# Kernel optimization log

Measured on AMD Instinct MI355X. Metric: run time of the kernel, lower is better.

Reference implementation:

```python
import jax, jax.numpy as jnp
import numpy as np

N = 4096   # out_features (rows of W)
M = 4096   # in_features (cols of W)
S_L = 2048 # Givens pairs on rows
S_R = 2048 # Givens pairs on cols
T = 8192   # tokens (batch*seq)
EPS = 1e-6


def _disjoint_pairs(key, n_feat, n_pairs):
    perm = jax.random.permutation(key, n_feat)[: 2 * n_pairs]
    return perm.reshape(n_pairs, 2).astype(jnp.int32)


def setup_inputs() -> dict:
    key = jax.random.key(0)
    ks = jax.random.split(key, 8)
    x = jax.random.normal(ks[0], (T, M), dtype=jnp.float32)
    W = 0.02 * jax.random.normal(ks[1], (N, M), dtype=jnp.float32)
    bias = jnp.zeros((N,), dtype=jnp.float32)
    theta_L = 0.002 * jax.random.normal(ks[2], (S_L,), dtype=jnp.float32)
    theta_R = 0.002 * jax.random.normal(ks[3], (S_R,), dtype=jnp.float32)
    pairs_L = _disjoint_pairs(ks[4], N, S_L)
    pairs_R = _disjoint_pairs(ks[5], M, S_R)
    ecd_log_mag = jnp.zeros((N,), dtype=jnp.float32)
    base_row_norms = jnp.linalg.norm(W, axis=1)  # [N], captured at init
    return {"x": x, "W": W, "bias": bias, "theta_L": theta_L,
            "theta_R": theta_R, "ecd_log_mag": ecd_log_mag,
            "base_row_norms": base_row_norms, "pairs_L": pairs_L,
            "pairs_R": pairs_R}


def _rotate_rows(Wm, pairs, theta):
    # Disjoint Givens rotations on rows: gather pair rows, 2x2 rotate, scatter.
    i, j = pairs[:, 0], pairs[:, 1]
    c = jnp.cos(theta)[:, None]
    s = jnp.sin(theta)[:, None]
    ri, rj = Wm[i], Wm[j]              # [S, M] gathers
    return Wm.at[i].set(c * ri - s * rj).at[j].set(s * ri + c * rj)


def _rotate_cols(Wm, pairs, theta):
    i, j = pairs[:, 0], pairs[:, 1]
    c = jnp.cos(theta)[None, :]
    s = jnp.sin(theta)[None, :]
    ci, cj = Wm[:, i], Wm[:, j]        # [N, S] gathers
    return Wm.at[:, i].set(c * ci - s * cj).at[:, j].set(s * ci + c * cj)


def reference(x, W, bias, theta_L, theta_R, ecd_log_mag, base_row_norms,
              pairs_L, pairs_R):
    # Effective weight: W_eff = G_L(theta_L) @ W @ G_R(theta_R)^T
    W_eff = _rotate_rows(_rotate_cols(W, pairs_R, theta_R), pairs_L, theta_L)
    # Magnitude (ECD) rescaling: restore base per-row norms modulated by
    # learned log-magnitudes.
    row_norms = jnp.sqrt(jnp.sum(W_eff * W_eff, axis=1) + EPS)  # [N]
    scale = base_row_norms * jnp.exp(ecd_log_mag) / row_norms   # [N]
    W_eff = W_eff * scale[:, None]
    return x @ W_eff.T + bias
```

## Files before the change

kernel.cpp:

```cpp
#include <hip/hip_runtime.h>
#include <cstdint>
#include <cstddef>

constexpr int T_N = 8192;
constexpr int MM  = 4096;
constexpr int NN  = 4096;
constexpr int S_L = 2048;
constexpr int S_R = 2048;
constexpr float EPS_ = 1e-6f;

typedef float  f32x4  __attribute__((ext_vector_type(4)));
typedef __bf16 bf16x8 __attribute__((ext_vector_type(8)));
typedef unsigned short ushort8 __attribute__((ext_vector_type(8)));

__device__ __forceinline__ unsigned short f2bf(float f) {
  unsigned int u = __float_as_uint(f);
  u += 0x7FFFu + ((u >> 16) & 1u);
  return (unsigned short)(u >> 16);
}

__global__ void init_maps(float* rowC, float* rowS, int* rowP,
                          float* colC, float* colS, int* colP) {
  int i = blockIdx.x * blockDim.x + threadIdx.x;
  if (i < NN) { rowC[i] = 1.f; rowS[i] = 0.f; rowP[i] = i; }
  if (i < MM) { colC[i] = 1.f; colS[i] = 0.f; colP[i] = i; }
}

__global__ void build_maps(const float* __restrict__ thL, const float* __restrict__ thR,
                           const int* __restrict__ prL, const int* __restrict__ prR,
                           float* rowC, float* rowS, int* rowP,
                           float* colC, float* colS, int* colP) {
  int s = blockIdx.x * blockDim.x + threadIdx.x;
  if (s < S_L) {
    int i = prL[2*s], j = prL[2*s+1];
    float c = cosf(thL[s]), sn = sinf(thL[s]);
    rowC[i] = c; rowS[i] = -sn; rowP[i] = j;
    rowC[j] = c; rowS[j] =  sn; rowP[j] = i;
  }
  if (s < S_R) {
    int i = prR[2*s], j = prR[2*s+1];
    float c = cosf(thR[s]), sn = sinf(thR[s]);
    colC[i] = c; colS[i] = -sn; colP[i] = j;
    colC[j] = c; colS[j] =  sn; colP[j] = i;
  }
}

__global__ __launch_bounds__(256) void build_weff(
    const float* __restrict__ W, const float* __restrict__ brn, const float* __restrict__ elm,
    const float* __restrict__ rowC, const float* __restrict__ rowS, const int* __restrict__ rowP,
    const float* __restrict__ colC, const float* __restrict__ colS, const int* __restrict__ colP,
    unsigned short* __restrict__ Wb)
{
  __shared__ __align__(16) float rA[MM];
  __shared__ __align__(16) float rB[MM];
  __shared__ __align__(16) float rE[MM];
  __shared__ float red[4];

  int n   = blockIdx.x;
  int tid = threadIdx.x;
  int pn  = rowP[n];
  float cl = rowC[n], sl = rowS[n];
  const float* Wn = W + (size_t)n  * MM;
  const float* Wp = W + (size_t)pn * MM;

  for (int m = tid * 4; m < MM; m += 1024) {
    *(f32x4*)&rA[m] = *(const f32x4*)&Wn[m];
    *(f32x4*)&rB[m] = *(const f32x4*)&Wp[m];
  }
  __syncthreads();

  float ss = 0.f;
  for (int m = tid; m < MM; m += 256) {
    int p = colP[m];
    float c = colC[m], s = colS[m];
    float e = cl * (c * rA[m] + s * rA[p]) + sl * (c * rB[m] + s * rB[p]);
    rE[m] = e;
    ss += e * e;
  }
  #pragma unroll
  for (int o = 32; o; o >>= 1) ss += __shfl_xor(ss, o);
  int lane = tid & 63, wid = tid >> 6;
  if (lane == 0) red[wid] = ss;
  __syncthreads();
  float tot = red[0] + red[1] + red[2] + red[3];
  float scale = brn[n] * expf(elm[n]) / sqrtf(tot + EPS_);

  for (int m = tid * 8; m < MM; m += 2048) {
    ushort8 pkt;
    #pragma unroll
    for (int q = 0; q < 8; q++) pkt[q] = f2bf(rE[m + q] * scale);
    *(ushort8*)&Wb[(size_t)n * MM + m] = pkt;
  }
}

__global__ __launch_bounds__(256) void conv_x(const float* __restrict__ x,
                                              unsigned short* __restrict__ xb) {
  const size_t total = (size_t)T_N * MM / 8;
  for (size_t i = (size_t)blockIdx.x * 256 + threadIdx.x; i < total; i += 2048ull * 256ull) {
    const float* s = x + i * 8;
    f32x4 v0 = *(const f32x4*)s;
    f32x4 v1 = *(const f32x4*)(s + 4);
    ushort8 p;
    p[0] = f2bf(v0.x); p[1] = f2bf(v0.y); p[2] = f2bf(v0.z); p[3] = f2bf(v0.w);
    p[4] = f2bf(v1.x); p[5] = f2bf(v1.y); p[6] = f2bf(v1.z); p[7] = f2bf(v1.w);
    *(ushort8*)(xb + i * 8) = p;
  }
}

typedef const __attribute__((address_space(1))) unsigned int* as1_u32p;
typedef __attribute__((address_space(3))) unsigned int* as3_u32p;

__device__ __forceinline__ void gl_lds16(const void* g, void* l) {
  __builtin_amdgcn_global_load_lds((as1_u32p)g, (as3_u32p)l, 16, 0, 0);
}

constexpr int GBM = 256, GBN = 256, GBK = 64;
constexpr int NTK = MM / GBK;
constexpr int ASLOT = GBM * GBK * 2;
constexpr int BSLOT = GBN * GBK * 2;

#define SB0() __builtin_amdgcn_sched_barrier(0)
#define LGKM(N) do { asm volatile("s_waitcnt lgkmcnt(" #N ")" ::: "memory"); \
                     SB0(); } while (0)

#define RD_BP(NI0, BB)                                                        \
  _Pragma("unroll") for (int n_ = 0; n_ < 2; ++n_)                            \
  _Pragma("unroll") for (int k_ = 0; k_ < 2; ++k_)                            \
    bf[(NI0) + n_][k_] = *(const bf16x8*)((BB) + brow0 + ((NI0) + n_) * 2048  \
                                           + ((k_ * 64 + lg * 16) ^ sw));

#define RD_AQ(DST, AB, Q)                                                     \
  _Pragma("unroll") for (int i_ = 0; i_ < 2; ++i_)                            \
  _Pragma("unroll") for (int k_ = 0; k_ < 2; ++k_)                            \
    DST[i_][k_] = *(const bf16x8*)((AB) + arow0 + ((Q) * 2 + i_) * 2048       \
                                    + ((k_ * 64 + lg * 16) ^ sw));

#define CL(AF, Q, H)                                                          \
  __builtin_amdgcn_s_setprio(1);                                              \
  _Pragma("unroll") for (int k_ = 0; k_ < 2; ++k_)                            \
  _Pragma("unroll") for (int i_ = 0; i_ < 2; ++i_)                            \
  _Pragma("unroll") for (int n_ = 0; n_ < 2; ++n_)                            \
    acc[(Q) * 2 + i_][(H) + n_] = __builtin_amdgcn_mfma_f32_16x16x32_bf16(    \
        AF[i_][k_], bf[(H) + n_][k_], acc[(Q) * 2 + i_][(H) + n_], 0, 0, 0);  \
  __builtin_amdgcn_s_setprio(0);

#define STAGE_A(KOF, SL)                                                      \
  _Pragma("unroll") for (int l_ = 0; l_ < 4; ++l_)                            \
    gl_lds16(sA + (size_t)l_ * (64 * MM) + (KOF),                             \
             ldsA + (SL) * ASLOT + dstb + l_ * 8192);
#define STAGE_B(KOF, SL)                                                      \
  _Pragma("unroll") for (int l_ = 0; l_ < 4; ++l_)                            \
    gl_lds16(sB + (size_t)l_ * (64 * MM) + (KOF),                             \
             ldsB + (SL) * BSLOT + dstb + l_ * 8192);

#define GATE4 do { asm volatile("s_waitcnt vmcnt(4)" ::: "memory");           \
                   __builtin_amdgcn_s_barrier(); } while (0)
#define GATE0 do { asm volatile("s_waitcnt vmcnt(0)" ::: "memory");           \
                   __builtin_amdgcn_s_barrier(); } while (0)
#define NOGATE do { } while (0)

#define TILE(KOF, RA, RB, WA, WB, DOB, DOA, GATE)                             \
  {                                                                           \
    const char* Ab_ = ldsA + (RA) * ASLOT;                                    \
    const char* Bb_ = ldsB + (RB) * BSLOT;                                    \
    bf16x8 bf[4][2], af0[2][2], af1[2][2], af2[2][2], af3[2][2];              \
    RD_BP(0, Bb_);                                                            \
    RD_AQ(af0, Ab_, 0);                                                       \
    SB0();                                                                    \
    RD_AQ(af1, Ab_, 1);                                                       \
    if (DOB) { STAGE_B((KOF) + GBK, WB); }                                    \
    SB0();                                                                    \
    if (DOA) { STAGE_A((KOF) + 2 * GBK, WA); }                                \
    LGKM(4);                                                                  \
    CL(af0, 0, 0);                                                   \
    RD_BP(2, Bb_);                                                            \
    LGKM(4);                                                                  \
    CL(af1, 1, 0);                                                   \
    RD_AQ(af2, Ab_, 2);                                                       \
    LGKM(4);                                                                  \
    CL(af0, 0, 2);                                                   \
    RD_AQ(af3, Ab_, 3);                                                       \
    LGKM(4);                                                                  \
    CL(af1, 1, 2);                                                   \
    CL(af2, 2, 0);                                                   \
    CL(af2, 2, 2);                                                   \
    LGKM(0);                                                                  \
    CL(af3, 3, 0);                                                   \
    CL(af3, 3, 2);                                                   \
    GATE;                                                                     \
  }

__global__ __launch_bounds__(512, 2) void gemm8(
    const unsigned short* __restrict__ xb,
    const unsigned short* __restrict__ wb,
    const float* __restrict__ bias,
    float* __restrict__ C)
{
  __shared__ __align__(16) unsigned short As[3 * GBM * GBK];
  __shared__ __align__(16) unsigned short Bs[2 * GBN * GBK];
  char* ldsA = (char*)As;
  char* ldsB = (char*)Bs;

  int bid = blockIdx.x;
  int swz = (bid & 7) * 64 + (bid >> 3);
  int tn = swz & 15, tm = swz >> 4;
  const int trow0 = tm * GBM;
  const int tcol0 = tn * GBN;

  int tid  = threadIdx.x;
  int lane = tid & 63;
  int wid  = tid >> 6;
  int wr = wid >> 2, wc = wid & 3;
  int lr = lane & 15;
  int lg = lane >> 4;
  const int sw = (lr & 7) << 4;
  const int arow0 = wr * 16384 + lr * 128;
  const int brow0 = wc * 8192  + lr * 128;

  const int r0   = tid >> 3;
  const int colg = (tid & 7) ^ (r0 & 7);
  const unsigned short* sA = xb + (size_t)(trow0 + r0) * MM + colg * 8;
  const unsigned short* sB = wb + (size_t)(tcol0 + r0) * MM + colg * 8;
  const int dstb = tid * 16;

  f32x4 acc[8][4];
  #pragma unroll
  for (int i = 0; i < 8; i++)
    #pragma unroll
    for (int j = 0; j < 4; j++) {
      f32x4 z = {0.f, 0.f, 0.f, 0.f};
      acc[i][j] = z;
    }

  STAGE_B(0, 0);
  STAGE_A(0, 0);
  SB0();
  STAGE_B(GBK, 1);
  STAGE_A(GBK, 1);
  STAGE_A(2 * GBK, 2);
  asm volatile("s_waitcnt vmcnt(12)" ::: "memory");
  __builtin_amdgcn_s_barrier();

  int kof = 0;
  #pragma unroll 1
  for (int tb = 0; tb < NTK - 4; tb += 6) {
    TILE(kof      , 0, 0, 2, 1, 1, 1, GATE4);
    TILE(kof +  64, 1, 1, 0, 0, 1, 1, GATE4);
    TILE(kof + 128, 2, 0, 1, 1, 1, 1, GATE4);
    TILE(kof + 192, 0, 1, 2, 0, 1, 1, GATE4);
    TILE(kof + 256, 1, 0, 0, 1, 1, 1, GATE4);
    TILE(kof + 320, 2, 1, 1, 0, 1, 1, GATE4);
    kof += 384;
  }
  TILE(kof      , 0, 0, 2, 1, 1, 1, GATE4);
  TILE(kof +  64, 1, 1, 0, 0, 1, 1, GATE4);
  TILE(kof + 128, 2, 0, 0, 1, 1, 0, GATE0);
  TILE(kof + 192, 0, 1, 0, 0, 0, 0, NOGATE);

  #pragma unroll
  for (int ni = 0; ni < 4; ++ni) {
    int col = tcol0 + wc * 64 + ni * 16 + lr;
    float bi = bias[col];
    #pragma unroll
    for (int mi = 0; mi < 8; ++mi) {
      int rr0 = trow0 + wr * 128 + mi * 16 + lg * 4;
      #pragma unroll
      for (int qq = 0; qq < 4; ++qq)
        C[(size_t)(rr0 + qq) * NN + col] = acc[mi][ni][qq] + bi;
    }
  }
}

constexpr int BM = 128, BN = 128, BK = 64;

__global__ __launch_bounds__(256) void gemm_fb(
    const float* __restrict__ xf,
    const unsigned short* __restrict__ wb, const float* __restrict__ bias,
    float* __restrict__ C)
{
  __shared__ __align__(16) unsigned short As2[BM * BK];
  __shared__ __align__(16) unsigned short Bs2[BN * BK];

  int bid = blockIdx.x;
  int swz = (bid & 7) * 256 + (bid >> 3);
  int tn = swz & 31;
  int tm = swz >> 5;

  int tid  = threadIdx.x;
  int lane = tid & 63;
  int wid  = tid >> 6;
  int wr = wid >> 1, wc = wid & 1;
  int lr = lane & 15;
  int lg = lane >> 4;

  f32x4 acc[4][4];
  #pragma unroll
  for (int i = 0; i < 4; i++)
    #pragma unroll
    for (int j = 0; j < 4; j++) {
      f32x4 z = {0.f, 0.f, 0.f, 0.f};
      acc[i][j] = z;
    }

  int srow = tid >> 3;
  int scol = (tid & 7) * 8;
  const size_t a_base = (size_t)(tm * BM) * MM;
  const size_t b_base = (size_t)(tn * BN) * MM;

  for (int k0 = 0; k0 < MM; k0 += BK) {
    #pragma unroll
    for (int c = 0; c < 4; c++) {
      int row = c * 32 + srow;
      gl_lds16(wb + b_base + (size_t)row * MM + k0 + scol,
               (char*)Bs2 + (c * 256 + wid * 64) * 16);
    }
    #pragma unroll
    for (int c = 0; c < 4; c++) {
      int row = c * 32 + srow;
      const float* s = xf + a_base + (size_t)row * MM + k0 + scol;
      f32x4 v0 = *(const f32x4*)s;
      f32x4 v1 = *(const f32x4*)(s + 4);
      ushort8 p;
      p[0] = f2bf(v0.x); p[1] = f2bf(v0.y); p[2] = f2bf(v0.z); p[3] = f2bf(v0.w);
      p[4] = f2bf(v1.x); p[5] = f2bf(v1.y); p[6] = f2bf(v1.z); p[7] = f2bf(v1.w);
      *(ushort8*)&As2[(c * 256 + tid) * 8] = p;
    }
    __syncthreads();

    #pragma unroll
    for (int kk = 0; kk < 2; kk++) {
      bf16x8 a[4], b[4];
      #pragma unroll
      for (int i = 0; i < 4; i++) {
        a[i] = *(const bf16x8*)&As2[(wr * 64 + i * 16 + lr) * BK + kk * 32 + lg * 8];
        b[i] = *(const bf16x8*)&Bs2[(wc * 64 + i * 16 + lr) * BK + kk * 32 + lg * 8];
      }
      #pragma unroll
      for (int i = 0; i < 4; i++)
        #pragma unroll
        for (int j = 0; j < 4; j++)
          acc[i][j] = __builtin_amdgcn_mfma_f32_16x16x32_bf16(a[i], b[j], acc[i][j], 0, 0, 0);
    }
    __syncthreads();
  }

  int gn0 = tn * BN + wc * 64;
  int gt0 = tm * BM + wr * 64;
  #pragma unroll
  for (int j = 0; j < 4; j++) {
    int gn = gn0 + j * 16 + lr;
    float bi = bias[gn];
    #pragma unroll
    for (int i = 0; i < 4; i++) {
      int t0 = gt0 + i * 16 + lg * 4;
      #pragma unroll
      for (int q = 0; q < 4; q++)
        C[(size_t)(t0 + q) * NN + gn] = acc[i][j][q] + bi;
    }
  }
}

extern "C" void kernel_launch(void* const* d_in, const int* in_sizes, int n_in,
                              void* d_out, int out_size, void* d_ws, size_t ws_size,
                              hipStream_t stream)
{
  const float* x    = (const float*)d_in[0];
  const float* W    = (const float*)d_in[1];
  const float* bias = (const float*)d_in[2];
  const float* thL  = (const float*)d_in[3];
  const float* thR  = (const float*)d_in[4];
  const float* elm  = (const float*)d_in[5];
  const float* brn  = (const float*)d_in[6];
  const int*   prL  = (const int*)d_in[7];
  const int*   prR  = (const int*)d_in[8];
  float* out = (float*)d_out;

  char* ws = (char*)d_ws;
  unsigned short* Wb = (unsigned short*)ws;
  size_t off = (size_t)NN * MM * 2;
  float* rowC = (float*)(ws + off); off += NN * 4;
  float* rowS = (float*)(ws + off); off += NN * 4;
  int*   rowP = (int*)  (ws + off); off += NN * 4;
  float* colC = (float*)(ws + off); off += MM * 4;
  float* colS = (float*)(ws + off); off += MM * 4;
  int*   colP = (int*)  (ws + off); off += MM * 4;
  unsigned short* xb = (unsigned short*)(ws + off);
  bool use_xb = ws_size >= off + (size_t)T_N * MM * 2;

  init_maps <<<16, 256, 0, stream>>>(rowC, rowS, rowP, colC, colS, colP);
  build_maps<<< 8, 256, 0, stream>>>(thL, thR, prL, prR, rowC, rowS, rowP, colC, colS, colP);
  build_weff<<<NN, 256, 0, stream>>>(W, brn, elm, rowC, rowS, rowP, colC, colS, colP, Wb);

  if (use_xb) {
    conv_x<<<2048, 256, 0, stream>>>(x, xb);
    gemm8<<<512, 512, 0, stream>>>(xb, Wb, bias, out);
  } else {
    gemm_fb<<<2048, 256, 0, stream>>>(x, Wb, bias, out);
  }
}
```

Before: 325.4 us.

## Switch bf16 GEMM to 32x32x16 MFMA tiles and drop redundant prologue loads

The main GEMM's 16x16x32 MFMA fragments become 32x32x16 MFMA fragments. The LDS read addressing, swizzle offsets, accumulator layout and epilogue store mapping are reworked to match. The larger instruction halves the MFMA issue count per tile and gives 32-wide contiguous column stores in the epilogue. The prologue no longer issues B/A stages that the first tile issues again, and the vmcnt wait is adjusted to match. It risks new LDS bank-conflict patterns from the changed swizzle and a different latency/dependency profile in the interleaved schedule.

```diff
diff --git a/kernel.cpp b/kernel.cpp
--- a/kernel.cpp
+++ b/kernel.cpp
@@ -9,8 +9,9 @@
 constexpr int S_R = 2048;
 constexpr float EPS_ = 1e-6f;
 
-typedef float  f32x4  __attribute__((ext_vector_type(4)));
-typedef __bf16 bf16x8 __attribute__((ext_vector_type(8)));
+typedef float  f32x4   __attribute__((ext_vector_type(4)));
+typedef float  f32x16  __attribute__((ext_vector_type(16)));
+typedef __bf16 bf16x8  __attribute__((ext_vector_type(8)));
 typedef unsigned short ushort8 __attribute__((ext_vector_type(8)));
 
 __device__ __forceinline__ unsigned short f2bf(float f) {
@@ -123,25 +124,20 @@
 #define LGKM(N) do { asm volatile("s_waitcnt lgkmcnt(" #N ")" ::: "memory"); \
                      SB0(); } while (0)
 
-#define RD_BP(NI0, BB)                                                        \
+#define RD_B8(BB)                                                             \
   _Pragma("unroll") for (int n_ = 0; n_ < 2; ++n_)                            \
-  _Pragma("unroll") for (int k_ = 0; k_ < 2; ++k_)                            \
-    bf[(NI0) + n_][k_] = *(const bf16x8*)((BB) + brow0 + ((NI0) + n_) * 2048  \
-                                           + ((k_ * 64 + lg * 16) ^ sw));
-
-#define RD_AQ(DST, AB, Q)                                                     \
-  _Pragma("unroll") for (int i_ = 0; i_ < 2; ++i_)                            \
-  _Pragma("unroll") for (int k_ = 0; k_ < 2; ++k_)                            \
-    DST[i_][k_] = *(const bf16x8*)((AB) + arow0 + ((Q) * 2 + i_) * 2048       \
-                                    + ((k_ * 64 + lg * 16) ^ sw));
-
-#define CL(AF, Q, H)                                                          \
+  _Pragma("unroll") for (int k_ = 0; k_ < 4; ++k_)                            \
+    bf[n_][k_] = *(const bf16x8*)((BB) + brow0 + n_ * 4096 + koff[k_]);
+
+#define RD_A4(DST, AB, MB)                                                    \
+  _Pragma("unroll") for (int k_ = 0; k_ < 4; ++k_)                            \
+    DST[k_] = *(const bf16x8*)((AB) + arow0 + (MB) * 4096 + koff[k_]);
+
+#define CL4(AF, MB, NB)                                                       \
   __builtin_amdgcn_s_setprio(1);                                              \
-  _Pragma("unroll") for (int k_ = 0; k_ < 2; ++k_)                            \
-  _Pragma("unroll") for (int i_ = 0; i_ < 2; ++i_)                            \
-  _Pragma("unroll") for (int n_ = 0; n_ < 2; ++n_)                            \
-    acc[(Q) * 2 + i_][(H) + n_] = __builtin_amdgcn_mfma_f32_16x16x32_bf16(    \
-        AF[i_][k_], bf[(H) + n_][k_], acc[(Q) * 2 + i_][(H) + n_], 0, 0, 0);  \
+  _Pragma("unroll") for (int k_ = 0; k_ < 4; ++k_)                            \
+    acc[MB][NB] = __builtin_amdgcn_mfma_f32_32x32x16_bf16(                    \
+        AF[k_], bf[NB][k_], acc[MB][NB], 0, 0, 0);                            \
   __builtin_amdgcn_s_setprio(0);
 
 #define STAGE_A(KOF, SL)                                                      \
@@ -163,30 +159,29 @@
   {                                                                           \
     const char* Ab_ = ldsA + (RA) * ASLOT;                                    \
     const char* Bb_ = ldsB + (RB) * BSLOT;                                    \
-    bf16x8 bf[4][2], af0[2][2], af1[2][2], af2[2][2], af3[2][2];              \
-    RD_BP(0, Bb_);                                                            \
-    RD_AQ(af0, Ab_, 0);                                                       \
+    bf16x8 bf[2][4], af0[4], af1[4], af2[4], af3[4];                          \
+    RD_B8(Bb_);                                                               \
+    RD_A4(af0, Ab_, 0);                                                       \
     SB0();                                                                    \
-    RD_AQ(af1, Ab_, 1);                                                       \
+    RD_A4(af1, Ab_, 1);                                                       \
+    SB0();                                                                    \
     if (DOB) { STAGE_B((KOF) + GBK, WB); }                                    \
     SB0();                                                                    \
     if (DOA) { STAGE_A((KOF) + 2 * GBK, WA); }                                \
     LGKM(4);                                                                  \
-    CL(af0, 0, 0);                                                   \
-    RD_BP(2, Bb_);                                                            \
+    CL4(af0, 0, 0);                                                           \
+    RD_A4(af2, Ab_, 2);                                                       \
     LGKM(4);                                                                  \
-    CL(af1, 1, 0);                                                   \
-    RD_AQ(af2, Ab_, 2);                                                       \
+    CL4(af1, 1, 0);                                                           \
+    CL4(af0, 0, 1);                                                           \
+    RD_A4(af3, Ab_, 3);                                                       \
     LGKM(4);                                                                  \
-    CL(af0, 0, 2);                                                   \
-    RD_AQ(af3, Ab_, 3);                                                       \
-    LGKM(4);                                                                  \
-    CL(af1, 1, 2);                                                   \
-    CL(af2, 2, 0);                                                   \
-    CL(af2, 2, 2);                                                   \
+    CL4(af2, 2, 0);                                                           \
+    CL4(af1, 1, 1);                                                           \
     LGKM(0);                                                                  \
-    CL(af3, 3, 0);                                                   \
-    CL(af3, 3, 2);                                                   \
+    CL4(af3, 3, 0);                                                           \
+    CL4(af2, 2, 1);                                                           \
+    CL4(af3, 3, 1);                                                           \
     GATE;                                                                     \
   }
 
@@ -211,11 +206,14 @@
   int lane = tid & 63;
   int wid  = tid >> 6;
   int wr = wid >> 2, wc = wid & 3;
-  int lr = lane & 15;
-  int lg = lane >> 4;
-  const int sw = (lr & 7) << 4;
-  const int arow0 = wr * 16384 + lr * 128;
-  const int brow0 = wc * 8192  + lr * 128;
+  int l31 = lane & 31;
+  int hi  = lane >> 5;
+  const int sw = (lane & 7) << 4;
+  const int arow0 = (wr * 128 + l31) * 128;
+  const int brow0 = (wc * 64  + l31) * 128;
+  int koff[4];
+  #pragma unroll
+  for (int k_ = 0; k_ < 4; ++k_) koff[k_] = (k_ * 32 + hi * 16) ^ sw;
 
   const int r0   = tid >> 3;
   const int colg = (tid & 7) ^ (r0 & 7);
@@ -223,22 +221,19 @@
   const unsigned short* sB = wb + (size_t)(tcol0 + r0) * MM + colg * 8;
   const int dstb = tid * 16;
 
-  f32x4 acc[8][4];
-  #pragma unroll
-  for (int i = 0; i < 8; i++)
-    #pragma unroll
-    for (int j = 0; j < 4; j++) {
-      f32x4 z = {0.f, 0.f, 0.f, 0.f};
-      acc[i][j] = z;
-    }
+  f32x16 acc[4][2];
+  #pragma unroll
+  for (int i = 0; i < 4; i++)
+    #pragma unroll
+    for (int j = 0; j < 2; j++)
+      #pragma unroll
+      for (int q = 0; q < 16; q++) acc[i][j][q] = 0.f;
 
   STAGE_B(0, 0);
   STAGE_A(0, 0);
   SB0();
-  STAGE_B(GBK, 1);
   STAGE_A(GBK, 1);
-  STAGE_A(2 * GBK, 2);
-  asm volatile("s_waitcnt vmcnt(12)" ::: "memory");
+  asm volatile("s_waitcnt vmcnt(4)" ::: "memory");
   __builtin_amdgcn_s_barrier();
 
   int kof = 0;
@@ -258,15 +253,17 @@
   TILE(kof + 192, 0, 1, 0, 0, 0, 0, NOGATE);
 
   #pragma unroll
-  for (int ni = 0; ni < 4; ++ni) {
-    int col = tcol0 + wc * 64 + ni * 16 + lr;
+  for (int nb = 0; nb < 2; ++nb) {
+    int col = tcol0 + wc * 64 + nb * 32 + l31;
     float bi = bias[col];
     #pragma unroll
-    for (int mi = 0; mi < 8; ++mi) {
-      int rr0 = trow0 + wr * 128 + mi * 16 + lg * 4;
-      #pragma unroll
-      for (int qq = 0; qq < 4; ++qq)
-        C[(size_t)(rr0 + qq) * NN + col] = acc[mi][ni][qq] + bi;
+    for (int mb = 0; mb < 4; ++mb) {
+      int row0 = trow0 + wr * 128 + mb * 32 + 4 * hi;
+      #pragma unroll
+      for (int rg = 0; rg < 16; ++rg) {
+        int row = row0 + (rg & 3) + 8 * (rg >> 2);
+        C[(size_t)row * NN + col] = acc[mb][nb][rg] + bi;
+      }
     }
   }
 }
```

After: 342.0 us. 5.1% more time.

## Process Givens row pairs per block and rework GEMM to double-buffered 8-wave pipeline

Applied to the files above, without the earlier changes.

The weight build now handles each left Givens pair in one block, loading both rows once and writing both rotated rows. This removes the row-map kernels and halves the W row reads, and it works because S_L*2 == N covers every row. The main GEMM drops from a triple-buffered A schedule to a double-buffered one, with larger per-wave fragment reads and more barriers between MFMA quarters. That changes the load/compute overlap and cuts LDS use, but the extra s_barriers may stall the waves.

```diff
diff --git a/kernel.cpp b/kernel.cpp
--- a/kernel.cpp
+++ b/kernel.cpp
@@ -9,8 +9,8 @@
 constexpr int S_R = 2048;
 constexpr float EPS_ = 1e-6f;
 
-typedef float  f32x4  __attribute__((ext_vector_type(4)));
-typedef __bf16 bf16x8 __attribute__((ext_vector_type(8)));
+typedef float  f32x4   __attribute__((ext_vector_type(4)));
+typedef __bf16 bf16x8  __attribute__((ext_vector_type(8)));
 typedef unsigned short ushort8 __attribute__((ext_vector_type(8)));
 
 __device__ __forceinline__ unsigned short f2bf(float f) {
@@ -19,24 +19,14 @@
   return (unsigned short)(u >> 16);
 }
 
-__global__ void init_maps(float* rowC, float* rowS, int* rowP,
-                          float* colC, float* colS, int* colP) {
+__global__ void init_cols(float* colC, float* colS, int* colP) {
   int i = blockIdx.x * blockDim.x + threadIdx.x;
-  if (i < NN) { rowC[i] = 1.f; rowS[i] = 0.f; rowP[i] = i; }
   if (i < MM) { colC[i] = 1.f; colS[i] = 0.f; colP[i] = i; }
 }
 
-__global__ void build_maps(const float* __restrict__ thL, const float* __restrict__ thR,
-                           const int* __restrict__ prL, const int* __restrict__ prR,
-                           float* rowC, float* rowS, int* rowP,
+__global__ void build_cols(const float* __restrict__ thR, const int* __restrict__ prR,
                            float* colC, float* colS, int* colP) {
   int s = blockIdx.x * blockDim.x + threadIdx.x;
-  if (s < S_L) {
-    int i = prL[2*s], j = prL[2*s+1];
-    float c = cosf(thL[s]), sn = sinf(thL[s]);
-    rowC[i] = c; rowS[i] = -sn; rowP[i] = j;
-    rowC[j] = c; rowS[j] =  sn; rowP[j] = i;
-  }
   if (s < S_R) {
     int i = prR[2*s], j = prR[2*s+1];
     float c = cosf(thR[s]), sn = sinf(thR[s]);
@@ -45,51 +35,64 @@
   }
 }
 
-__global__ __launch_bounds__(256) void build_weff(
+__global__ __launch_bounds__(256) void weff_pair(
     const float* __restrict__ W, const float* __restrict__ brn, const float* __restrict__ elm,
-    const float* __restrict__ rowC, const float* __restrict__ rowS, const int* __restrict__ rowP,
+    const float* __restrict__ thL, const int* __restrict__ prL,
     const float* __restrict__ colC, const float* __restrict__ colS, const int* __restrict__ colP,
     unsigned short* __restrict__ Wb)
 {
-  __shared__ __align__(16) float rA[MM];
-  __shared__ __align__(16) float rB[MM];
-  __shared__ __align__(16) float rE[MM];
-  __shared__ float red[4];
-
-  int n   = blockIdx.x;
+  __shared__ __align__(16) float rI[MM];
+  __shared__ __align__(16) float rJ[MM];
+  __shared__ float red[8];
+
+  int s   = blockIdx.x;
   int tid = threadIdx.x;
-  int pn  = rowP[n];
-  float cl = rowC[n], sl = rowS[n];
-  const float* Wn = W + (size_t)n  * MM;
-  const float* Wp = W + (size_t)pn * MM;
+  int i = prL[2*s], j = prL[2*s+1];
+  float cl = cosf(thL[s]), sl = sinf(thL[s]);
+  const float* Wi = W + (size_t)i * MM;
+  const float* Wj = W + (size_t)j * MM;
 
   for (int m = tid * 4; m < MM; m += 1024) {
-    *(f32x4*)&rA[m] = *(const f32x4*)&Wn[m];
-    *(f32x4*)&rB[m] = *(const f32x4*)&Wp[m];
+    *(f32x4*)&rI[m] = *(const f32x4*)&Wi[m];
+    *(f32x4*)&rJ[m] = *(const f32x4*)&Wj[m];
   }
   __syncthreads();
 
-  float ss = 0.f;
+  float ssi = 0.f, ssj = 0.f;
   for (int m = tid; m < MM; m += 256) {
     int p = colP[m];
-    float c = colC[m], s = colS[m];
-    float e = cl * (c * rA[m] + s * rA[p]) + sl * (c * rB[m] + s * rB[p]);
-    rE[m] = e;
-    ss += e * e;
-  }
-  #pragma unroll
-  for (int o = 32; o; o >>= 1) ss += __shfl_xor(ss, o);
+    float c = colC[m], sn = colS[m];
+    float vi = c * rI[m] + sn * rI[p];
+    float vj = c * rJ[m] + sn * rJ[p];
+    float ei = cl * vi - sl * vj;
+    float ej = sl * vi + cl * vj;
+    ssi += ei * ei;
+    ssj += ej * ej;
+  }
+  #pragma unroll
+  for (int o = 32; o; o >>= 1) { ssi += __shfl_xor(ssi, o); ssj += __shfl_xor(ssj, o); }
   int lane = tid & 63, wid = tid >> 6;
-  if (lane == 0) red[wid] = ss;
+  if (lane == 0) { red[wid] = ssi; red[4 + wid] = ssj; }
   __syncthreads();
-  float tot = red[0] + red[1] + red[2] + red[3];
-  float scale = brn[n] * expf(elm[n]) / sqrtf(tot + EPS_);
-
-  for (int m = tid * 8; m < MM; m += 2048) {
-    ushort8 pkt;
-    #pragma unroll
-    for (int q = 0; q < 8; q++) pkt[q] = f2bf(rE[m + q] * scale);
-    *(ushort8*)&Wb[(size_t)n * MM + m] = pkt;
+  float ti = red[0] + red[1] + red[2] + red[3];
+  float tj = red[4] + red[5] + red[6] + red[7];
+  float sci = brn[i] * expf(elm[i]) / sqrtf(ti + EPS_);
+  float scj = brn[j] * expf(elm[j]) / sqrtf(tj + EPS_);
+
+  for (int m0 = tid * 8; m0 < MM; m0 += 2048) {
+    ushort8 pi, pj;
+    #pragma unroll
+    for (int q = 0; q < 8; q++) {
+      int m = m0 + q;
+      int p = colP[m];
+      float c = colC[m], sn = colS[m];
+      float vi = c * rI[m] + sn * rI[p];
+      float vj = c * rJ[m] + sn * rJ[p];
+      pi[q] = f2bf((cl * vi - sl * vj) * sci);
+      pj[q] = f2bf((sl * vi + cl * vj) * scj);
+    }
+    *(ushort8*)&Wb[(size_t)i * MM + m0] = pi;
+    *(ushort8*)&Wb[(size_t)j * MM + m0] = pj;
   }
 }
 
@@ -116,78 +119,81 @@
 
 constexpr int GBM = 256, GBN = 256, GBK = 64;
 constexpr int NTK = MM / GBK;
-constexpr int ASLOT = GBM * GBK * 2;
-constexpr int BSLOT = GBN * GBK * 2;
+constexpr int BUFB = GBM * GBK * 2;
 
 #define SB0() __builtin_amdgcn_sched_barrier(0)
+#define BAR() __builtin_amdgcn_s_barrier()
 #define LGKM(N) do { asm volatile("s_waitcnt lgkmcnt(" #N ")" ::: "memory"); \
                      SB0(); } while (0)
 
-#define RD_BP(NI0, BB)                                                        \
+#define RD_A8(DST, AB, MIH)                                                   \
+  _Pragma("unroll") for (int i_ = 0; i_ < 4; ++i_)                            \
+  _Pragma("unroll") for (int k_ = 0; k_ < 2; ++k_)                            \
+    DST[i_][k_] = *(const bf16x8*)((AB) + arow0 + ((MIH) * 4 + i_) * 2048     \
+                                    + ((k_ * 64 + lg * 16) ^ sw));
+
+#define RD_B4(DST, BB, NIH)                                                   \
   _Pragma("unroll") for (int n_ = 0; n_ < 2; ++n_)                            \
   _Pragma("unroll") for (int k_ = 0; k_ < 2; ++k_)                            \
-    bf[(NI0) + n_][k_] = *(const bf16x8*)((BB) + brow0 + ((NI0) + n_) * 2048  \
-                                           + ((k_ * 64 + lg * 16) ^ sw));
-
-#define RD_AQ(DST, AB, Q)                                                     \
-  _Pragma("unroll") for (int i_ = 0; i_ < 2; ++i_)                            \
-  _Pragma("unroll") for (int k_ = 0; k_ < 2; ++k_)                            \
-    DST[i_][k_] = *(const bf16x8*)((AB) + arow0 + ((Q) * 2 + i_) * 2048       \
+    DST[n_][k_] = *(const bf16x8*)((BB) + brow0 + ((NIH) * 2 + n_) * 2048     \
                                     + ((k_ * 64 + lg * 16) ^ sw));
 
-#define CL(AF, Q, H)                                                          \
+#define QMF(AF, BF, MI0, NI0)                                                 \
   __builtin_amdgcn_s_setprio(1);                                              \
   _Pragma("unroll") for (int k_ = 0; k_ < 2; ++k_)                            \
-  _Pragma("unroll") for (int i_ = 0; i_ < 2; ++i_)                            \
+  _Pragma("unroll") for (int i_ = 0; i_ < 4; ++i_)                            \
   _Pragma("unroll") for (int n_ = 0; n_ < 2; ++n_)                            \
-    acc[(Q) * 2 + i_][(H) + n_] = __builtin_amdgcn_mfma_f32_16x16x32_bf16(    \
-        AF[i_][k_], bf[(H) + n_][k_], acc[(Q) * 2 + i_][(H) + n_], 0, 0, 0);  \
+    acc[(MI0) + i_][(NI0) + n_] = __builtin_amdgcn_mfma_f32_16x16x32_bf16(    \
+        AF[i_][k_], BF[n_][k_], acc[(MI0) + i_][(NI0) + n_], 0, 0, 0);        \
   __builtin_amdgcn_s_setprio(0);
 
-#define STAGE_A(KOF, SL)                                                      \
-  _Pragma("unroll") for (int l_ = 0; l_ < 4; ++l_)                            \
+#define STG_A(KOF, BUF, H)                                                    \
+  _Pragma("unroll") for (int l_ = 2 * (H); l_ < 2 * (H) + 2; ++l_)            \
     gl_lds16(sA + (size_t)l_ * (64 * MM) + (KOF),                             \
-             ldsA + (SL) * ASLOT + dstb + l_ * 8192);
-#define STAGE_B(KOF, SL)                                                      \
-  _Pragma("unroll") for (int l_ = 0; l_ < 4; ++l_)                            \
+             ldsA + (BUF) * BUFB + dstb + l_ * 8192);
+#define STG_B(KOF, BUF, H)                                                    \
+  _Pragma("unroll") for (int l_ = 2 * (H); l_ < 2 * (H) + 2; ++l_)            \
     gl_lds16(sB + (size_t)l_ * (64 * MM) + (KOF),                             \
-             ldsB + (SL) * BSLOT + dstb + l_ * 8192);
-
-#define GATE4 do { asm volatile("s_waitcnt vmcnt(4)" ::: "memory");           \
-                   __builtin_amdgcn_s_barrier(); } while (0)
-#define GATE0 do { asm volatile("s_waitcnt vmcnt(0)" ::: "memory");           \
-                   __builtin_amdgcn_s_barrier(); } while (0)
-#define NOGATE do { } while (0)
-
-#define TILE(KOF, RA, RB, WA, WB, DOB, DOA, GATE)                             \
+             ldsB + (BUF) * BUFB + dstb + l_ * 8192);
+
+#define GATE6  asm volatile("s_waitcnt vmcnt(6)" ::: "memory")
+#define GATE0v asm volatile("s_waitcnt vmcnt(0)" ::: "memory")
+#define GNONE  do { } while (0)
+
+#define TILE8(T, BB, DOB1, DOA2, GATEK)                                       \
   {                                                                           \
-    const char* Ab_ = ldsA + (RA) * ASLOT;                                    \
-    const char* Bb_ = ldsB + (RB) * BSLOT;                                    \
-    bf16x8 bf[4][2], af0[2][2], af1[2][2], af2[2][2], af3[2][2];              \
-    RD_BP(0, Bb_);                                                            \
-    RD_AQ(af0, Ab_, 0);                                                       \
-    SB0();                                                                    \
-    RD_AQ(af1, Ab_, 1);                                                       \
-    if (DOB) { STAGE_B((KOF) + GBK, WB); }                                    \
-    SB0();                                                                    \
-    if (DOA) { STAGE_A((KOF) + 2 * GBK, WA); }                                \
-    LGKM(4);                                                                  \
-    CL(af0, 0, 0);                                                   \
-    RD_BP(2, Bb_);                                                            \
-    LGKM(4);                                                                  \
-    CL(af1, 1, 0);                                                   \
-    RD_AQ(af2, Ab_, 2);                                                       \
-    LGKM(4);                                                                  \
-    CL(af0, 0, 2);                                                   \
-    RD_AQ(af3, Ab_, 3);                                                       \
-    LGKM(4);                                                                  \
-    CL(af1, 1, 2);                                                   \
-    CL(af2, 2, 0);                                                   \
-    CL(af2, 2, 2);                                                   \
+    const char* Ab_ = ldsA + (BB) * BUFB;                                     \
+    const char* Bb_ = ldsB + (BB) * BUFB;                                     \
+    bf16x8 afA[4][2], afB[4][2], bfA[2][2], bfB[2][2];                        \
+           \
+    RD_A8(afA, Ab_, 0);                                                       \
+    RD_B4(bfA, Bb_, 0);                                                       \
+    if (DOB1) { STG_B(((T) + 1) * GBK, (BB) ^ 1, 1); }                        \
+    LGKM(8);                                                                  \
+    BAR();                                                                    \
     LGKM(0);                                                                  \
-    CL(af3, 3, 0);                                                   \
-    CL(af3, 3, 2);                                                   \
-    GATE;                                                                     \
+    QMF(afA, bfA, 0, 0);                                                      \
+    BAR();                                                                    \
+                                         \
+    RD_A8(afB, Ab_, 1);                                                       \
+    BAR();                                                                    \
+    LGKM(0);                                                                  \
+    QMF(afB, bfA, 4, 0);                                                      \
+    BAR();                                                                    \
+                          \
+    RD_B4(bfB, Bb_, 1);                                                       \
+    if (DOA2) { STG_A(((T) + 2) * GBK, (BB), 0); }                            \
+    BAR();                                                                    \
+    LGKM(0);                                                                  \
+    QMF(afB, bfB, 4, 2);                                                      \
+    BAR();                                                                    \
+               \
+    if (DOA2) { STG_A(((T) + 2) * GBK, (BB), 1);                              \
+                STG_B(((T) + 2) * GBK, (BB), 0); }                            \
+    GATEK;                                                                    \
+    BAR();                                                                    \
+    QMF(afA, bfB, 0, 2);                                                      \
+    BAR();                                                                    \
   }
 
 __global__ __launch_bounds__(512, 2) void gemm8(
@@ -196,7 +202,7 @@
     const float* __restrict__ bias,
     float* __restrict__ C)
 {
-  __shared__ __align__(16) unsigned short As[3 * GBM * GBK];
+  __shared__ __align__(16) unsigned short As[2 * GBM * GBK];
   __shared__ __align__(16) unsigned short Bs[2 * GBN * GBK];
   char* ldsA = (char*)As;
   char* ldsB = (char*)Bs;
@@ -214,8 +220,8 @@
   int lr = lane & 15;
   int lg = lane >> 4;
   const int sw = (lr & 7) << 4;
-  const int arow0 = wr * 16384 + lr * 128;
-  const int brow0 = wc * 8192  + lr * 128;
+  const int arow0 = (wr * 128 + lr) * 128;
+  const int brow0 = (wc * 64  + lr) * 128;
 
   const int r0   = tid >> 3;
   const int colg = (tid & 7) ^ (r0 & 7);
@@ -232,30 +238,18 @@
       acc[i][j] = z;
     }
 
-  STAGE_B(0, 0);
-  STAGE_A(0, 0);
-  SB0();
-  STAGE_B(GBK, 1);
-  STAGE_A(GBK, 1);
-  STAGE_A(2 * GBK, 2);
-  asm volatile("s_waitcnt vmcnt(12)" ::: "memory");
+  STG_A(0, 0, 0); STG_A(0, 0, 1); STG_B(0, 0, 0); STG_B(0, 0, 1);
+  STG_A(GBK, 1, 0); STG_A(GBK, 1, 1); STG_B(GBK, 1, 0);
+  asm volatile("s_waitcnt vmcnt(6)" ::: "memory");
   __builtin_amdgcn_s_barrier();
 
-  int kof = 0;
   #pragma unroll 1
-  for (int tb = 0; tb < NTK - 4; tb += 6) {
-    TILE(kof      , 0, 0, 2, 1, 1, 1, GATE4);
-    TILE(kof +  64, 1, 1, 0, 0, 1, 1, GATE4);
-    TILE(kof + 128, 2, 0, 1, 1, 1, 1, GATE4);
-    TILE(kof + 192, 0, 1, 2, 0, 1, 1, GATE4);
-    TILE(kof + 256, 1, 0, 0, 1, 1, 1, GATE4);
-    TILE(kof + 320, 2, 1, 1, 0, 1, 1, GATE4);
-    kof += 384;
-  }
-  TILE(kof      , 0, 0, 2, 1, 1, 1, GATE4);
-  TILE(kof +  64, 1, 1, 0, 0, 1, 1, GATE4);
-  TILE(kof + 128, 2, 0, 0, 1, 1, 0, GATE0);
-  TILE(kof + 192, 0, 1, 0, 0, 0, 0, NOGATE);
+  for (int t = 0; t < NTK - 2; t += 2) {
+    TILE8(t,     0, 1, 1, GATE6);
+    TILE8(t + 1, 1, 1, 1, GATE6);
+  }
+  TILE8(NTK - 2, 0, 1, 0, GATE0v);
+  TILE8(NTK - 1, 1, 0, 0, GNONE);
 
   #pragma unroll
   for (int ni = 0; ni < 4; ++ni) {
@@ -378,18 +372,15 @@
   char* ws = (char*)d_ws;
   unsigned short* Wb = (unsigned short*)ws;
   size_t off = (size_t)NN * MM * 2;
-  float* rowC = (float*)(ws + off); off += NN * 4;
-  float* rowS = (float*)(ws + off); off += NN * 4;
-  int*   rowP = (int*)  (ws + off); off += NN * 4;
   float* colC = (float*)(ws + off); off += MM * 4;
   float* colS = (float*)(ws + off); off += MM * 4;
   int*   colP = (int*)  (ws + off); off += MM * 4;
   unsigned short* xb = (unsigned short*)(ws + off);
   bool use_xb = ws_size >= off + (size_t)T_N * MM * 2;
 
-  init_maps <<<16, 256, 0, stream>>>(rowC, rowS, rowP, colC, colS, colP);
-  build_maps<<< 8, 256, 0, stream>>>(thL, thR, prL, prR, rowC, rowS, rowP, colC, colS, colP);
-  build_weff<<<NN, 256, 0, stream>>>(W, brn, elm, rowC, rowS, rowP, colC, colS, colP, Wb);
+  init_cols <<<16, 256, 0, stream>>>(colC, colS, colP);
+  build_cols<<< 8, 256, 0, stream>>>(thR, prR, colC, colS, colP);
+  weff_pair <<<S_L, 256, 0, stream>>>(W, brn, elm, thL, prL, colC, colS, colP, Wb);
 
   if (use_xb) {
     conv_x<<<2048, 256, 0, stream>>>(x, xb);
```

Result: no change. 320.4 us (-1.6%).
